# Performance work log

Hardware: AMD Instinct MI355X
Metric: run time of the kernel (lower is better)

## Reference

```python
import jax, jax.numpy as jnp
import numpy as np

N = 50000      # nodes
E = 800000     # edges (avg in-degree ~16)
IN = 64        # in_size
OUT = 64       # out_size
DELTA = 2.83   # PNA delta ~ log(avg_degree + 1)
MOM_EPS = 1e-30
BN_EPS = 1e-5


def setup_inputs() -> dict:
    key = jax.random.key(0)
    ks = jax.random.split(key, 8)
    node_feat = jax.random.normal(ks[0], (N, IN), dtype=jnp.float32)
    # Linear M: (2*IN -> IN); store weight as (2*IN, IN) for x @ W
    Wm = jax.random.normal(ks[1], (2 * IN, IN), dtype=jnp.float32) * (1.0 / np.sqrt(2 * IN))
    bm = jnp.zeros((IN,), jnp.float32)
    # Linear U: ((4 aggs * 3 scalers + 1) * IN -> OUT) = (13*IN -> OUT)
    Wu = jax.random.normal(ks[2], (13 * IN, OUT), dtype=jnp.float32) * (1.0 / np.sqrt(13 * IN))
    bu = jnp.zeros((OUT,), jnp.float32)
    gamma = jnp.ones((OUT,), jnp.float32)
    beta = jnp.zeros((OUT,), jnp.float32)
    src = jax.random.randint(ks[3], (E,), 0, N, dtype=jnp.int32)
    dst = jax.random.randint(ks[4], (E,), 0, N, dtype=jnp.int32)
    return {"node_feat": node_feat, "Wm": Wm, "bm": bm, "Wu": Wu, "bu": bu,
            "gamma": gamma, "beta": beta, "src": src, "dst": dst}


def _pna_forward(node_feat, Wm, bm, Wu, bu, gamma, beta, src, dst):
    # message MLP: M(h_src || h_dst) computed without materializing the concat
    msg = node_feat[src] @ Wm[:IN] + node_feat[dst] @ Wm[IN:] + bm  # (E, IN)

    deg = jax.ops.segment_sum(jnp.ones((E,), msg.dtype), dst, num_segments=N)  # (N,)
    safe_deg = jnp.maximum(deg, 1.0)[:, None]
    has_nbr = (deg > 0.0)[:, None]

    # multi-statistic ragged segment reduce
    s = jax.ops.segment_sum(msg, dst, num_segments=N)
    mean = s / safe_deg
    mean_sq = jax.ops.segment_sum(msg * msg, dst, num_segments=N) / safe_deg
    var = jax.nn.relu(mean_sq - mean * mean)
    std = jnp.sqrt(var + MOM_EPS)
    mx = jnp.where(has_nbr, jax.ops.segment_max(msg, dst, num_segments=N), 0.0)
    mn = jnp.where(has_nbr, jax.ops.segment_min(msg, dst, num_segments=N), 0.0)

    h = jnp.concatenate([mean, mx, mn, std], axis=1)  # (N, 4*IN)

    # scalers: identity, amplification log(D+1)/delta, attenuation delta/log(D+1)
    logD = jnp.log(deg + 1.0)[:, None]
    safe_logD = jnp.where(logD > 0.0, logD, 1.0)  # zero-degree rows masked below
    h_all = jnp.concatenate([h, h * (safe_logD / DELTA), h * (DELTA / safe_logD)], axis=1)
    h_neigh = jnp.where(has_nbr, h_all, 0.0)  # zero-degree nodes get 0 (DGL behavior)

    # update MLP + graph size norm (single graph: snorm = 1/sqrt(N))
    z = jnp.concatenate([node_feat, h_neigh], axis=1) @ Wu + bu  # (N, OUT)
    snorm = 1.0 / jnp.sqrt(jnp.asarray(N, z.dtype))
    z = z * snorm

    # BatchNorm1d, training mode (batch stats, biased variance)
    mu = jnp.mean(z, axis=0)
    v = jnp.mean((z - mu) ** 2, axis=0)
    return (z - mu) / jnp.sqrt(v + BN_EPS) * gamma + beta


def reference(node_feat, Wm, bm, Wu, bu, gamma, beta, src, dst):
    return _pna_forward(node_feat, Wm, bm, Wu, bu, gamma, beta, src, dst)
```

## Files before the change

### kernel.cpp

```cpp
#include <hip/hip_runtime.h>
#include <hip/hip_bf16.h>


#define DELTA_C 2.83f
#define BN_EPS_C 1e-5f
#define MOM_EPS_C 1e-30f
#define FLT_BIG 3.402823466e38f
#define BSHIFT 7
#define NBMAX 512

typedef __attribute__((ext_vector_type(8))) short bf16x8;
typedef __attribute__((ext_vector_type(4))) float f32x4;

static __device__ __forceinline__ unsigned short f2bf(float f) {
    unsigned u = __float_as_uint(f);
    unsigned r = (u + 0x7FFFu + ((u >> 16) & 1u)) >> 16;
    return (unsigned short)r;
}
static __device__ __forceinline__ unsigned pack2(float a, float b) {
    return (unsigned)f2bf(a) | ((unsigned)f2bf(b) << 16);
}
static __device__ __forceinline__ float bflo(unsigned u) { return __uint_as_float(u << 16); }
static __device__ __forceinline__ float bfhi(unsigned u) { return __uint_as_float(u & 0xFFFF0000u); }

__global__ __launch_bounds__(256) void repack_wu(
    const float* __restrict__ Wu, short* __restrict__ Wup,
    int* __restrict__ bcnt, float* __restrict__ bnacc)
{
    int t = threadIdx.x;
    if (blockIdx.x == 0) {
        bcnt[t] = 0; bcnt[t + 256] = 0;
        if (t < 128) bnacc[t] = 0.f;
    }
    int idx = blockIdx.x * 256 + t;
    int lane = idx & 63, c = (idx >> 6) & 3, kc = idx >> 8;
    int kbase = kc * 32 + (lane >> 4) * 8;
    int col = c * 16 + (lane & 15);
    unsigned short o[8];
    #pragma unroll
    for (int i = 0; i < 8; ++i)
        o[i] = f2bf(Wu[(size_t)(kbase + i) * 64 + col]);
    uint4 u;
    u.x = o[0] | ((unsigned)o[1] << 16);
    u.y = o[2] | ((unsigned)o[3] << 16);
    u.z = o[4] | ((unsigned)o[5] << 16);
    u.w = o[6] | ((unsigned)o[7] << 16);
    *(uint4*)(Wup + (size_t)idx * 8) = u;
}

__global__ __launch_bounds__(256) void proj_ab(
    const float* __restrict__ x, const float* __restrict__ Wm,
    unsigned* __restrict__ Ab, float* __restrict__ B,
    unsigned* __restrict__ xbu, int n,
    const int* __restrict__ dst, int* __restrict__ bcnt, int e, int nb_chunk)
{
    __shared__ float wm[128][68];
    __shared__ float xs[64][68];
    __shared__ int h[NBMAX];
    int t = threadIdx.x;
    for (int i = t; i < 2048; i += 256) {
        int k = i >> 4, c4 = (i & 15) << 2;
        *(float4*)&wm[k][c4] = *(const float4*)&Wm[k * 64 + c4];
    }
    int row0 = blockIdx.x * 64;
    for (int i = t; i < 1024; i += 256) {
        int r = i >> 4, k4 = (i & 15) << 2;
        int row = row0 + r;
        float4 v = make_float4(0.f, 0.f, 0.f, 0.f);
        if (row < n) v = *(const float4*)&x[(size_t)row * 64 + k4];
        *(float4*)&xs[r][k4] = v;
    }
    __syncthreads();
    int tr = t >> 4, tc = t & 15, c0 = tc << 2;
    float a[4][4] = {}; float b[4][4] = {};
    #pragma unroll 8
    for (int k = 0; k < 64; ++k) {
        float4 wa = *(float4*)&wm[k][c0];
        float4 wb = *(float4*)&wm[64 + k][c0];
        #pragma unroll
        for (int i = 0; i < 4; ++i) {
            float xv = xs[tr * 4 + i][k];
            a[i][0] += xv * wa.x; a[i][1] += xv * wa.y; a[i][2] += xv * wa.z; a[i][3] += xv * wa.w;
            b[i][0] += xv * wb.x; b[i][1] += xv * wb.y; b[i][2] += xv * wb.z; b[i][3] += xv * wb.w;
        }
    }
    #pragma unroll
    for (int i = 0; i < 4; ++i) {
        int r = tr * 4 + i;
        int row = row0 + r;
        uint2 xp;
        xp.x = pack2(xs[r][c0], xs[r][c0 + 1]);
        xp.y = pack2(xs[r][c0 + 2], xs[r][c0 + 3]);
        *(uint2*)&xbu[(size_t)row * 32 + (c0 >> 1)] = xp;
        if (row < n) {
            uint2 ap;
            ap.x = pack2(a[i][0], a[i][1]);
            ap.y = pack2(a[i][2], a[i][3]);
            *(uint2*)&Ab[(size_t)row * 32 + (c0 >> 1)] = ap;
            *(float4*)&B[(size_t)row * 64 + c0] = make_float4(b[i][0], b[i][1], b[i][2], b[i][3]);
        }
    }
    if (blockIdx.x < nb_chunk) {
        __syncthreads();
        for (int bb = t; bb < NBMAX; bb += 256) h[bb] = 0;
        __syncthreads();
        int base = blockIdx.x * 4096;
        int cnt = min(4096, e - base);
        for (int i = t; i < cnt; i += 256)
            atomicAdd(&h[dst[base + i] >> BSHIFT], 1);
        __syncthreads();
        for (int bb = t; bb < NBMAX; bb += 256)
            if (h[bb]) atomicAdd(&bcnt[bb], h[bb]);
    }
}

__global__ void bin_scan(const int* __restrict__ bcnt, int* __restrict__ boff,
                         int* __restrict__ gcur, int nb,
                         int* __restrict__ offs, int n, int e)
{
    int t = threadIdx.x;
    int v[8]; int s = 0;
    #pragma unroll
    for (int j = 0; j < 8; ++j) {
        int b = t * 8 + j;
        v[j] = (b < nb) ? bcnt[b] : 0;
        s += v[j];
    }
    int inc = s;
    #pragma unroll
    for (int st = 1; st < 64; st <<= 1) {
        int u = __shfl_up(inc, st);
        if (t >= st) inc += u;
    }
    int ex = inc - s;
    #pragma unroll
    for (int j = 0; j < 8; ++j) {
        int b = t * 8 + j;
        if (b < nb) { boff[b] = ex; gcur[b] = ex; }
        ex += v[j];
    }
    if (t == 63) { boff[nb] = e; offs[n] = e; }
}

__global__ __launch_bounds__(256) void bin_scatter(
    const int* __restrict__ src, const int* __restrict__ dst,
    int* __restrict__ gcur, unsigned* __restrict__ pairs_out, int e)
{
    __shared__ int hcnt[NBMAX], hstart[NBMAX], hcur[NBMAX], gpos[NBMAX];
    __shared__ unsigned pairs[4096];
    int t = threadIdx.x;
    int base = blockIdx.x * 4096;
    int cnt = min(4096, e - base);
    for (int b = t; b < NBMAX; b += 256) hcnt[b] = 0;
    __syncthreads();

    int ls[16], ld[16];
    #pragma unroll
    for (int j = 0; j < 16; ++j) {
        int i = t + j * 256;
        ls[j] = 0; ld[j] = -1;
        if (i < cnt) {
            ls[j] = src[base + i];
            ld[j] = dst[base + i];
            atomicAdd(&hcnt[ld[j] >> BSHIFT], 1);
        }
    }
    __syncthreads();
    if (t < 64) {
        int v[8]; int s = 0;
        #pragma unroll
        for (int j = 0; j < 8; ++j) { v[j] = hcnt[t * 8 + j]; s += v[j]; }
        int inc = s;
        #pragma unroll
        for (int st = 1; st < 64; st <<= 1) {
            int u = __shfl_up(inc, st);
            if (t >= st) inc += u;
        }
        int ex = inc - s;
        #pragma unroll
        for (int j = 0; j < 8; ++j) {
            hstart[t * 8 + j] = ex;
            hcur[t * 8 + j] = ex;
            ex += v[j];
        }
    }
    __syncthreads();
    #pragma unroll
    for (int j = 0; j < 16; ++j) {
        if (ld[j] >= 0) {
            int pos = atomicAdd(&hcur[ld[j] >> BSHIFT], 1);
            pairs[pos] = ((unsigned)ls[j] << 16) | (unsigned)ld[j];
        }
    }
    __syncthreads();
    for (int b = t; b < NBMAX; b += 256) {
        int c = hcnt[b];
        if (c) gpos[b] = atomicAdd(&gcur[b], c);
    }
    __syncthreads();
    #pragma unroll
    for (int j = 0; j < 16; ++j) {
        int i = t + j * 256;
        if (i < cnt) {
            unsigned p = pairs[i];
            int b = (int)(p & 0xFFFFu) >> BSHIFT;
            pairs_out[gpos[b] + (i - hstart[b])] = p;
        }
    }
}

__global__ __launch_bounds__(128) void csr_fill(
    const unsigned* __restrict__ pairs, const int* __restrict__ boff,
    int* __restrict__ offs, int* __restrict__ csr, int n)
{
    __shared__ int hist[128], pref[128], cur[128];
    int b = blockIdx.x, t = threadIdx.x;
    int base = boff[b], cnt = boff[b + 1] - base;
    int node0 = b << BSHIFT;
    hist[t] = 0;
    __syncthreads();
    for (int i = t; i < cnt; i += 128)
        atomicAdd(&hist[pairs[base + i] & 127u], 1);
    __syncthreads();
    if (t < 64) {
        int v0 = hist[2 * t], v1 = hist[2 * t + 1];
        int s = v0 + v1, inc = s;
        #pragma unroll
        for (int st = 1; st < 64; st <<= 1) {
            int u = __shfl_up(inc, st);
            if (t >= st) inc += u;
        }
        int ex = inc - s;
        pref[2 * t] = ex;       cur[2 * t] = ex;
        pref[2 * t + 1] = ex + v0; cur[2 * t + 1] = ex + v0;
    }
    __syncthreads();
    int node = node0 + t;
    if (node < n) offs[node] = base + pref[t];
    for (int i = t; i < cnt; i += 128) {
        unsigned p = pairs[base + i];
        int pos = atomicAdd(&cur[p & 127u], 1);
        csr[base + pos] = (int)(p >> 16);
    }
}

__global__ __launch_bounds__(256) void node_reduce(
    const unsigned* __restrict__ Ab, const float* __restrict__ Bp,
    const float* __restrict__ bm,
    const int* __restrict__ offs, const int* __restrict__ csr,
    unsigned* __restrict__ hbu, float* __restrict__ s1, float* __restrict__ s2,
    int n, int npad)
{
    int wid = threadIdx.x >> 6;
    int lane = threadIdx.x & 63;
    int node = blockIdx.x * 4 + wid;
    if (node >= npad) return;
    unsigned* hrow = hbu + (size_t)node * 128;
    int l32 = lane & 31;
    int half = lane >> 5;
    int beg = 0, dg = 0;
    if (node < n) { beg = offs[node]; dg = offs[node + 1] - beg; }
    if (dg == 0) {
        if (half == 0) {
            hrow[l32] = 0u; hrow[32 + l32] = 0u; hrow[64 + l32] = 0u; hrow[96 + l32] = 0u;
        }
        if (lane == 0) { s1[node] = 0.f; s2[node] = 0.f; }
        return;
    }

    float s0 = 0.f, s1a = 0.f, ss0 = 0.f, ss1 = 0.f;
    float mx0 = -FLT_BIG, mx1 = -FLT_BIG, mn0 = FLT_BIG, mn1 = FLT_BIG;

#define ACC(u) { float v0 = bflo(u), v1 = bfhi(u);                          \
    s0 += v0; s1a += v1;                                                    \
    ss0 = fmaf(v0, v0, ss0); ss1 = fmaf(v1, v1, ss1);                       \
    mx0 = fmaxf(mx0, v0); mx1 = fmaxf(mx1, v1);                             \
    mn0 = fminf(mn0, v0); mn1 = fminf(mn1, v1); }
#define GA(sel) Ab[(size_t)(sel) * 32 + l32]

    int j = beg, end = beg + dg;
    for (; j + 15 < end; j += 16) {
        int i0 = csr[j],      i1 = csr[j + 1],  i2 = csr[j + 2],  i3 = csr[j + 3];
        int i4 = csr[j + 4],  i5 = csr[j + 5],  i6 = csr[j + 6],  i7 = csr[j + 7];
        int i8 = csr[j + 8],  i9 = csr[j + 9],  i10 = csr[j + 10], i11 = csr[j + 11];
        int i12 = csr[j + 12], i13 = csr[j + 13], i14 = csr[j + 14], i15 = csr[j + 15];
        unsigned u0 = GA(half ? i1 : i0);
        unsigned u1 = GA(half ? i3 : i2);
        unsigned u2 = GA(half ? i5 : i4);
        unsigned u3 = GA(half ? i7 : i6);
        unsigned u4 = GA(half ? i9 : i8);
        unsigned u5 = GA(half ? i11 : i10);
        unsigned u6 = GA(half ? i13 : i12);
        unsigned u7 = GA(half ? i15 : i14);
        ACC(u0); ACC(u1); ACC(u2); ACC(u3);
        ACC(u4); ACC(u5); ACC(u6); ACC(u7);
    }
    for (; j + 7 < end; j += 8) {
        int i0 = csr[j],     i1 = csr[j + 1], i2 = csr[j + 2], i3 = csr[j + 3];
        int i4 = csr[j + 4], i5 = csr[j + 5], i6 = csr[j + 6], i7 = csr[j + 7];
        unsigned u0 = GA(half ? i1 : i0);
        unsigned u1 = GA(half ? i3 : i2);
        unsigned u2 = GA(half ? i5 : i4);
        unsigned u3 = GA(half ? i7 : i6);
        ACC(u0); ACC(u1); ACC(u2); ACC(u3);
    }
    for (; j + 1 < end; j += 2) {
        int i0 = csr[j], i1 = csr[j + 1];
        unsigned u0 = GA(half ? i1 : i0);
        ACC(u0);
    }
    if (j < end) {
        unsigned u0 = GA(csr[j]);
        if (half == 0) ACC(u0);
    }
#undef GA
#undef ACC

    s0 += __shfl_xor(s0, 32);  s1a += __shfl_xor(s1a, 32);
    ss0 += __shfl_xor(ss0, 32); ss1 += __shfl_xor(ss1, 32);
    mx0 = fmaxf(mx0, __shfl_xor(mx0, 32)); mx1 = fmaxf(mx1, __shfl_xor(mx1, 32));
    mn0 = fminf(mn0, __shfl_xor(mn0, 32)); mn1 = fminf(mn1, __shfl_xor(mn1, 32));

    float fd = (float)dg, inv = 1.0f / fd;
    float2 bv = *(const float2*)(Bp + (size_t)node * 64 + 2 * l32);
    float2 bmv = *(const float2*)(bm + 2 * l32);
    float bn0 = bv.x + bmv.x, bn1 = bv.y + bmv.y;
    float ma0 = s0 * inv, ma1 = s1a * inv;
    float var0 = ss0 * inv - ma0 * ma0; if (var0 < 0.f) var0 = 0.f;
    float var1 = ss1 * inv - ma1 * ma1; if (var1 < 0.f) var1 = 0.f;
    float sd0 = sqrtf(var0 + MOM_EPS_C), sd1 = sqrtf(var1 + MOM_EPS_C);

    if (half == 0) {
        hrow[l32]      = pack2(ma0 + bn0, ma1 + bn1);
        hrow[32 + l32] = pack2(mx0 + bn0, mx1 + bn1);
        hrow[64 + l32] = pack2(mn0 + bn0, mn1 + bn1);
        hrow[96 + l32] = pack2(sd0, sd1);
    }
    if (lane == 0) {
        float logD = logf(fd + 1.0f);
        s1[node] = logD / DELTA_C;
        s2[node] = DELTA_C / logD;
    }
}

__global__ __launch_bounds__(256) void gemm_mfma(
    const short* __restrict__ xb, const short* __restrict__ hb,
    const float* __restrict__ s1p, const float* __restrict__ s2p,
    const short* __restrict__ Wup, const float* __restrict__ bu,
    float* __restrict__ z, float* __restrict__ bnacc, int n, float snorm)
{
    __shared__ float bnl[4][2][64];
    int t = threadIdx.x;
    int lane = t & 63, w = t >> 6;
    int rb = blockIdx.x * 128 + w * 32;
    int r16 = lane & 15, kg = lane >> 4;

    f32x4 accx[2][4] = {};
    f32x4 acc1[2][4] = {};
    f32x4 acc2[2][4] = {};
    f32x4 acc3[2][4] = {};

    const short* xr0 = xb + (size_t)(rb + r16) * 64 + kg * 8;
    const short* xr1 = xr0 + 16 * 64;

    #pragma unroll
    for (int kc = 0; kc < 2; ++kc) {
        bf16x8 a0 = *(const bf16x8*)(xr0 + kc * 32);
        bf16x8 a1 = *(const bf16x8*)(xr1 + kc * 32);
        #pragma unroll
        for (int c = 0; c < 4; ++c) {
            bf16x8 b = *(const bf16x8*)(Wup + (size_t)((kc * 4 + c) * 64 + lane) * 8);
            accx[0][c] = __builtin_amdgcn_mfma_f32_16x16x32_bf16(a0, b, accx[0][c], 0, 0, 0);
            accx[1][c] = __builtin_amdgcn_mfma_f32_16x16x32_bf16(a1, b, accx[1][c], 0, 0, 0);
        }
    }

    const short* hr0 = hb + (size_t)(rb + r16) * 256 + kg * 8;
    const short* hr1 = hr0 + 16 * 256;

    #pragma unroll 1
    for (int kh = 0; kh < 8; ++kh) {
        bf16x8 a0 = *(const bf16x8*)(hr0 + kh * 32);
        bf16x8 a1 = *(const bf16x8*)(hr1 + kh * 32);
        #pragma unroll
        for (int c = 0; c < 4; ++c) {
            bf16x8 b1 = *(const bf16x8*)(Wup + (size_t)(((2  + kh) * 4 + c) * 64 + lane) * 8);
            bf16x8 b2 = *(const bf16x8*)(Wup + (size_t)(((10 + kh) * 4 + c) * 64 + lane) * 8);
            bf16x8 b3 = *(const bf16x8*)(Wup + (size_t)(((18 + kh) * 4 + c) * 64 + lane) * 8);
            acc1[0][c] = __builtin_amdgcn_mfma_f32_16x16x32_bf16(a0, b1, acc1[0][c], 0, 0, 0);
            acc1[1][c] = __builtin_amdgcn_mfma_f32_16x16x32_bf16(a1, b1, acc1[1][c], 0, 0, 0);
            acc2[0][c] = __builtin_amdgcn_mfma_f32_16x16x32_bf16(a0, b2, acc2[0][c], 0, 0, 0);
            acc2[1][c] = __builtin_amdgcn_mfma_f32_16x16x32_bf16(a1, b2, acc2[1][c], 0, 0, 0);
            acc3[0][c] = __builtin_amdgcn_mfma_f32_16x16x32_bf16(a0, b3, acc3[0][c], 0, 0, 0);
            acc3[1][c] = __builtin_amdgcn_mfma_f32_16x16x32_bf16(a1, b3, acc3[1][c], 0, 0, 0);
        }
    }

    float cs[4] = {}, css[4] = {};
    #pragma unroll
    for (int s = 0; s < 2; ++s) {
        int r0 = rb + s * 16 + kg * 4;
        float s1v[4], s2v[4];
        #pragma unroll
        for (int r = 0; r < 4; ++r) { s1v[r] = s1p[r0 + r]; s2v[r] = s2p[r0 + r]; }
        #pragma unroll
        for (int c = 0; c < 4; ++c) {
            int col = c * 16 + r16;
            float bval = bu[col];
            #pragma unroll
            for (int r = 0; r < 4; ++r) {
                int row = r0 + r;
                if (row < n) {
                    float v = (accx[s][c][r] + acc1[s][c][r]
                            + s1v[r] * acc2[s][c][r] + s2v[r] * acc3[s][c][r] + bval) * snorm;
                    z[(size_t)row * 64 + col] = v;
                    cs[c] += v;
                    css[c] = fmaf(v, v, css[c]);
                }
            }
        }
    }
    #pragma unroll
    for (int c = 0; c < 4; ++c) {
        float a = cs[c];  a += __shfl_xor(a, 16); a += __shfl_xor(a, 32); cs[c] = a;
        float b = css[c]; b += __shfl_xor(b, 16); b += __shfl_xor(b, 32); css[c] = b;
    }
    if (lane < 16) {
        #pragma unroll
        for (int c = 0; c < 4; ++c) {
            bnl[w][0][c * 16 + lane] = cs[c];
            bnl[w][1][c * 16 + lane] = css[c];
        }
    }
    __syncthreads();
    if (t < 128) {
        int st = t >> 6, cc = t & 63;
        float tot = bnl[0][st][cc] + bnl[1][st][cc] + bnl[2][st][cc] + bnl[3][st][cc];
        atomicAdd(&bnacc[st * 64 + cc], tot);
    }
}

__global__ __launch_bounds__(256) void bn_apply(
    float* __restrict__ z, const float* __restrict__ acc,
    const float* __restrict__ gamma, const float* __restrict__ beta, int n)
{
    float inv_n = 1.0f / (float)n;
    int tid = blockIdx.x * 256 + threadIdx.x;
    int c0 = (tid * 4) & 63;
    float sc[4], sh[4];
    #pragma unroll
    for (int k = 0; k < 4; ++k) {
        int c = c0 + k;
        float mu = acc[c] * inv_n;
        float var = acc[64 + c] * inv_n - mu * mu;
        if (var < 0.f) var = 0.f;
        float inv = rsqrtf(var + BN_EPS_C) * gamma[c];
        sc[k] = inv;
        sh[k] = beta[c] - mu * inv;
    }
    int total4 = n * 16;
    int stride = gridDim.x * 256;
    for (int i = tid; i < total4; i += stride) {
        float4 v = *(float4*)&z[(size_t)i * 4];
        v.x = fmaf(v.x, sc[0], sh[0]);
        v.y = fmaf(v.y, sc[1], sh[1]);
        v.z = fmaf(v.z, sc[2], sh[2]);
        v.w = fmaf(v.w, sc[3], sh[3]);
        *(float4*)&z[(size_t)i * 4] = v;
    }
}

extern "C" void kernel_launch(void* const* d_in, const int* in_sizes, int n_in,
                              void* d_out, int out_size, void* d_ws, size_t ws_size,
                              hipStream_t stream)
{
    const float* x     = (const float*)d_in[0];
    const float* Wm    = (const float*)d_in[1];
    const float* bm    = (const float*)d_in[2];
    const float* Wu    = (const float*)d_in[3];
    const float* bu    = (const float*)d_in[4];
    const float* gamma = (const float*)d_in[5];
    const float* beta  = (const float*)d_in[6];
    const int*   src   = (const int*)d_in[7];
    const int*   dst   = (const int*)d_in[8];

    int n = in_sizes[0] / 64;
    int e = in_sizes[7];
    int npad = ((n + 127) / 128) * 128;
    int nb = (n + 127) >> BSHIFT;
    float* z = (float*)d_out;

    char* w = (char*)d_ws;
    size_t off = 0;
    auto take = [&](size_t bytes) -> void* {
        void* p = w + off;
        off = (off + bytes + 255) & ~(size_t)255;
        return p;
    };
    unsigned* Ab    = (unsigned*)take((size_t)npad * 32 * sizeof(unsigned));
    float*    B     = (float*)take((size_t)n * 64 * sizeof(float));
    unsigned* xbu   = (unsigned*)take((size_t)npad * 32 * sizeof(unsigned));
    unsigned* hbu   = (unsigned*)take((size_t)npad * 128 * sizeof(unsigned));
    float*    s1    = (float*)take((size_t)npad * sizeof(float));
    float*    s2    = (float*)take((size_t)npad * sizeof(float));
    short*    Wup   = (short*)take((size_t)26 * 4 * 64 * 8 * sizeof(short));
    int*      offs  = (int*)take((size_t)(n + 1) * sizeof(int));
    int*      csr   = (int*)take((size_t)e * sizeof(int));
    unsigned* prs   = (unsigned*)take((size_t)e * sizeof(unsigned));
    int*      bcnt  = (int*)take((size_t)NBMAX * sizeof(int));
    int*      boff  = (int*)take((size_t)(NBMAX + 1) * sizeof(int));
    int*      gcur  = (int*)take((size_t)NBMAX * sizeof(int));
    float*    bnacc = (float*)take(128 * sizeof(float));

    (void)n_in; (void)out_size; (void)ws_size;

    int nb_rows64 = npad / 64;
    int nb_chunk = (e + 4095) / 4096;

    repack_wu<<<26, 256, 0, stream>>>(Wu, Wup, bcnt, bnacc);
    proj_ab<<<nb_rows64, 256, 0, stream>>>(x, Wm, Ab, B, xbu, n, dst, bcnt, e, nb_chunk);
    bin_scan<<<1, 64, 0, stream>>>(bcnt, boff, gcur, nb, offs, n, e);
    bin_scatter<<<nb_chunk, 256, 0, stream>>>(src, dst, gcur, prs, e);
    csr_fill<<<nb, 128, 0, stream>>>(prs, boff, offs, csr, n);
    node_reduce<<<(npad + 3) / 4, 256, 0, stream>>>(Ab, B, bm, offs, csr, hbu, s1, s2, n, npad);

    float snorm = (float)(1.0 / sqrt((double)n));
    gemm_mfma<<<npad / 128, 256, 0, stream>>>((const short*)xbu, (const short*)hbu,
                                              s1, s2, Wup, bu, z, bnacc, n, snorm);

    bn_apply<<<512, 256, 0, stream>>>(z, bnacc, gamma, beta, n);
}
```

Before: 123.3 us.

## Fold bin scan into scatter/fill kernels and widen node_reduce gathers to 16B

Removes the single-block bin_scan launch: bin_scatter now computes the bin prefix sums redundantly per block from bcnt, and gcur becomes a zero-initialized relative cursor. csr_fill computes its base offset by summing the preceding bin counts and writes the final offs entry itself. node_reduce is restructured so each lane loads a uint4 (8 bf16 values) per neighbor, with 8 neighbors handled concurrently per wavefront, followed by a cross-group shuffle reduction. This trades one kernel launch and narrow 4-byte gathers for redundant scan work in every block and more registers per thread.

```diff
diff --git a/kernel.cpp b/kernel.cpp
--- a/kernel.cpp
+++ b/kernel.cpp
@@ -25,11 +25,12 @@
 
 __global__ __launch_bounds__(256) void repack_wu(
     const float* __restrict__ Wu, short* __restrict__ Wup,
-    int* __restrict__ bcnt, float* __restrict__ bnacc)
+    int* __restrict__ bcnt, int* __restrict__ gcur, float* __restrict__ bnacc)
 {
     int t = threadIdx.x;
     if (blockIdx.x == 0) {
         bcnt[t] = 0; bcnt[t + 256] = 0;
+        gcur[t] = 0; gcur[t + 256] = 0;
         if (t < 128) bnacc[t] = 0.f;
     }
     int idx = blockIdx.x * 256 + t;
@@ -114,44 +115,37 @@
     }
 }
 
-__global__ void bin_scan(const int* __restrict__ bcnt, int* __restrict__ boff,
-                         int* __restrict__ gcur, int nb,
-                         int* __restrict__ offs, int n, int e)
-{
-    int t = threadIdx.x;
-    int v[8]; int s = 0;
-    #pragma unroll
-    for (int j = 0; j < 8; ++j) {
-        int b = t * 8 + j;
-        v[j] = (b < nb) ? bcnt[b] : 0;
-        s += v[j];
-    }
-    int inc = s;
-    #pragma unroll
-    for (int st = 1; st < 64; st <<= 1) {
-        int u = __shfl_up(inc, st);
-        if (t >= st) inc += u;
-    }
-    int ex = inc - s;
-    #pragma unroll
-    for (int j = 0; j < 8; ++j) {
-        int b = t * 8 + j;
-        if (b < nb) { boff[b] = ex; gcur[b] = ex; }
-        ex += v[j];
-    }
-    if (t == 63) { boff[nb] = e; offs[n] = e; }
-}
-
 __global__ __launch_bounds__(256) void bin_scatter(
     const int* __restrict__ src, const int* __restrict__ dst,
-    int* __restrict__ gcur, unsigned* __restrict__ pairs_out, int e)
-{
-    __shared__ int hcnt[NBMAX], hstart[NBMAX], hcur[NBMAX], gpos[NBMAX];
+    const int* __restrict__ bcnt, int* __restrict__ gcur,
+    unsigned* __restrict__ pairs_out, int e)
+{
+    __shared__ int hcnt[NBMAX], hstart[NBMAX], hcur[NBMAX], gpos[NBMAX], sgoff[NBMAX];
     __shared__ unsigned pairs[4096];
     int t = threadIdx.x;
     int base = blockIdx.x * 4096;
     int cnt = min(4096, e - base);
     for (int b = t; b < NBMAX; b += 256) hcnt[b] = 0;
+    if (t < 64) {
+        int v0 = bcnt[t * 8],     v1 = bcnt[t * 8 + 1], v2 = bcnt[t * 8 + 2], v3 = bcnt[t * 8 + 3];
+        int v4 = bcnt[t * 8 + 4], v5 = bcnt[t * 8 + 5], v6 = bcnt[t * 8 + 6], v7 = bcnt[t * 8 + 7];
+        int s = v0 + v1 + v2 + v3 + v4 + v5 + v6 + v7;
+        int inc = s;
+        #pragma unroll
+        for (int st = 1; st < 64; st <<= 1) {
+            int u = __shfl_up(inc, st);
+            if (t >= st) inc += u;
+        }
+        int ex = inc - s;
+        sgoff[t * 8] = ex;         ex += v0;
+        sgoff[t * 8 + 1] = ex;     ex += v1;
+        sgoff[t * 8 + 2] = ex;     ex += v2;
+        sgoff[t * 8 + 3] = ex;     ex += v3;
+        sgoff[t * 8 + 4] = ex;     ex += v4;
+        sgoff[t * 8 + 5] = ex;     ex += v5;
+        sgoff[t * 8 + 6] = ex;     ex += v6;
+        sgoff[t * 8 + 7] = ex;
+    }
     __syncthreads();
 
     int ls[16], ld[16];
@@ -195,7 +189,7 @@
     __syncthreads();
     for (int b = t; b < NBMAX; b += 256) {
         int c = hcnt[b];
-        if (c) gpos[b] = atomicAdd(&gcur[b], c);
+        if (c) gpos[b] = sgoff[b] + atomicAdd(&gcur[b], c);
     }
     __syncthreads();
     #pragma unroll
@@ -210,15 +204,23 @@
 }
 
 __global__ __launch_bounds__(128) void csr_fill(
-    const unsigned* __restrict__ pairs, const int* __restrict__ boff,
-    int* __restrict__ offs, int* __restrict__ csr, int n)
-{
-    __shared__ int hist[128], pref[128], cur[128];
+    const unsigned* __restrict__ pairs, const int* __restrict__ bcnt,
+    int* __restrict__ offs, int* __restrict__ csr, int n, int e)
+{
+    __shared__ int hist[128], pref[128], cur[128], sbase[1];
     int b = blockIdx.x, t = threadIdx.x;
-    int base = boff[b], cnt = boff[b + 1] - base;
+    if (t < 64) {
+        int acc = 0;
+        for (int k = t; k < b; k += 64) acc += bcnt[k];
+        acc += __shfl_down(acc, 32); acc += __shfl_down(acc, 16);
+        acc += __shfl_down(acc, 8);  acc += __shfl_down(acc, 4);
+        acc += __shfl_down(acc, 2);  acc += __shfl_down(acc, 1);
+        if (t == 0) sbase[0] = acc;
+    }
+    hist[t] = 0;
+    __syncthreads();
+    int base = sbase[0], cnt = bcnt[b];
     int node0 = b << BSHIFT;
-    hist[t] = 0;
-    __syncthreads();
     for (int i = t; i < cnt; i += 128)
         atomicAdd(&hist[pairs[base + i] & 127u], 1);
     __syncthreads();
@@ -237,6 +239,7 @@
     __syncthreads();
     int node = node0 + t;
     if (node < n) offs[node] = base + pref[t];
+    if (b == gridDim.x - 1 && t == 0) offs[n] = e;
     for (int i = t; i < cnt; i += 128) {
         unsigned p = pairs[base + i];
         int pos = atomicAdd(&cur[p & 127u], 1);
@@ -256,87 +259,106 @@
     int node = blockIdx.x * 4 + wid;
     if (node >= npad) return;
     unsigned* hrow = hbu + (size_t)node * 128;
-    int l32 = lane & 31;
-    int half = lane >> 5;
+    int g = lane >> 3;
+    int q = lane & 7;
     int beg = 0, dg = 0;
     if (node < n) { beg = offs[node]; dg = offs[node + 1] - beg; }
     if (dg == 0) {
-        if (half == 0) {
-            hrow[l32] = 0u; hrow[32 + l32] = 0u; hrow[64 + l32] = 0u; hrow[96 + l32] = 0u;
+        if (lane < 8) {
+            uint4 zz = make_uint4(0u, 0u, 0u, 0u);
+            *(uint4*)&hrow[q * 4]      = zz;
+            *(uint4*)&hrow[32 + q * 4] = zz;
+            *(uint4*)&hrow[64 + q * 4] = zz;
+            *(uint4*)&hrow[96 + q * 4] = zz;
         }
         if (lane == 0) { s1[node] = 0.f; s2[node] = 0.f; }
         return;
     }
 
-    float s0 = 0.f, s1a = 0.f, ss0 = 0.f, ss1 = 0.f;
-    float mx0 = -FLT_BIG, mx1 = -FLT_BIG, mn0 = FLT_BIG, mn1 = FLT_BIG;
-
-#define ACC(u) { float v0 = bflo(u), v1 = bfhi(u);                          \
-    s0 += v0; s1a += v1;                                                    \
-    ss0 = fmaf(v0, v0, ss0); ss1 = fmaf(v1, v1, ss1);                       \
-    mx0 = fmaxf(mx0, v0); mx1 = fmaxf(mx1, v1);                             \
-    mn0 = fminf(mn0, v0); mn1 = fminf(mn1, v1); }
-#define GA(sel) Ab[(size_t)(sel) * 32 + l32]
+    float as0 = 0.f, as1 = 0.f, as2 = 0.f, as3 = 0.f, as4 = 0.f, as5 = 0.f, as6 = 0.f, as7 = 0.f;
+    float aq0 = 0.f, aq1 = 0.f, aq2 = 0.f, aq3 = 0.f, aq4 = 0.f, aq5 = 0.f, aq6 = 0.f, aq7 = 0.f;
+    float ax0 = -FLT_BIG, ax1 = -FLT_BIG, ax2 = -FLT_BIG, ax3 = -FLT_BIG,
+          ax4 = -FLT_BIG, ax5 = -FLT_BIG, ax6 = -FLT_BIG, ax7 = -FLT_BIG;
+    float am0 = FLT_BIG, am1 = FLT_BIG, am2 = FLT_BIG, am3 = FLT_BIG,
+          am4 = FLT_BIG, am5 = FLT_BIG, am6 = FLT_BIG, am7 = FLT_BIG;
+
+#define ACCP(u, S0, Q0, X0, M0, S1_, Q1_, X1_, M1_) {                         \
+    float v0 = bflo(u), v1 = bfhi(u);                                         \
+    S0 += v0; Q0 = fmaf(v0, v0, Q0); X0 = fmaxf(X0, v0); M0 = fminf(M0, v0);  \
+    S1_ += v1; Q1_ = fmaf(v1, v1, Q1_); X1_ = fmaxf(X1_, v1); M1_ = fminf(M1_, v1); }
+#define ACC8(V) {                                          \
+    ACCP((V).x, as0, aq0, ax0, am0, as1, aq1, ax1, am1);   \
+    ACCP((V).y, as2, aq2, ax2, am2, as3, aq3, ax3, am3);   \
+    ACCP((V).z, as4, aq4, ax4, am4, as5, aq5, ax5, am5);   \
+    ACCP((V).w, as6, aq6, ax6, am6, as7, aq7, ax7, am7); }
+#define GA4(idx) (((const uint4*)Ab)[(size_t)(idx) * 8 + q])
 
     int j = beg, end = beg + dg;
     for (; j + 15 < end; j += 16) {
-        int i0 = csr[j],      i1 = csr[j + 1],  i2 = csr[j + 2],  i3 = csr[j + 3];
-        int i4 = csr[j + 4],  i5 = csr[j + 5],  i6 = csr[j + 6],  i7 = csr[j + 7];
-        int i8 = csr[j + 8],  i9 = csr[j + 9],  i10 = csr[j + 10], i11 = csr[j + 11];
-        int i12 = csr[j + 12], i13 = csr[j + 13], i14 = csr[j + 14], i15 = csr[j + 15];
-        unsigned u0 = GA(half ? i1 : i0);
-        unsigned u1 = GA(half ? i3 : i2);
-        unsigned u2 = GA(half ? i5 : i4);
-        unsigned u3 = GA(half ? i7 : i6);
-        unsigned u4 = GA(half ? i9 : i8);
-        unsigned u5 = GA(half ? i11 : i10);
-        unsigned u6 = GA(half ? i13 : i12);
-        unsigned u7 = GA(half ? i15 : i14);
-        ACC(u0); ACC(u1); ACC(u2); ACC(u3);
-        ACC(u4); ACC(u5); ACC(u6); ACC(u7);
+        int ia = csr[j + g];
+        int ib = csr[j + 8 + g];
+        uint4 va = GA4(ia);
+        uint4 vb = GA4(ib);
+        ACC8(va); ACC8(vb);
     }
     for (; j + 7 < end; j += 8) {
-        int i0 = csr[j],     i1 = csr[j + 1], i2 = csr[j + 2], i3 = csr[j + 3];
-        int i4 = csr[j + 4], i5 = csr[j + 5], i6 = csr[j + 6], i7 = csr[j + 7];
-        unsigned u0 = GA(half ? i1 : i0);
-        unsigned u1 = GA(half ? i3 : i2);
-        unsigned u2 = GA(half ? i5 : i4);
-        unsigned u3 = GA(half ? i7 : i6);
-        ACC(u0); ACC(u1); ACC(u2); ACC(u3);
-    }
-    for (; j + 1 < end; j += 2) {
-        int i0 = csr[j], i1 = csr[j + 1];
-        unsigned u0 = GA(half ? i1 : i0);
-        ACC(u0);
+        int ia = csr[j + g];
+        uint4 va = GA4(ia);
+        ACC8(va);
     }
     if (j < end) {
-        unsigned u0 = GA(csr[j]);
-        if (half == 0) ACC(u0);
-    }
-#undef GA
-#undef ACC
-
-    s0 += __shfl_xor(s0, 32);  s1a += __shfl_xor(s1a, 32);
-    ss0 += __shfl_xor(ss0, 32); ss1 += __shfl_xor(ss1, 32);
-    mx0 = fmaxf(mx0, __shfl_xor(mx0, 32)); mx1 = fmaxf(mx1, __shfl_xor(mx1, 32));
-    mn0 = fminf(mn0, __shfl_xor(mn0, 32)); mn1 = fminf(mn1, __shfl_xor(mn1, 32));
-
-    float fd = (float)dg, inv = 1.0f / fd;
-    float2 bv = *(const float2*)(Bp + (size_t)node * 64 + 2 * l32);
-    float2 bmv = *(const float2*)(bm + 2 * l32);
-    float bn0 = bv.x + bmv.x, bn1 = bv.y + bmv.y;
-    float ma0 = s0 * inv, ma1 = s1a * inv;
-    float var0 = ss0 * inv - ma0 * ma0; if (var0 < 0.f) var0 = 0.f;
-    float var1 = ss1 * inv - ma1 * ma1; if (var1 < 0.f) var1 = 0.f;
-    float sd0 = sqrtf(var0 + MOM_EPS_C), sd1 = sqrtf(var1 + MOM_EPS_C);
-
-    if (half == 0) {
-        hrow[l32]      = pack2(ma0 + bn0, ma1 + bn1);
-        hrow[32 + l32] = pack2(mx0 + bn0, mx1 + bn1);
-        hrow[64 + l32] = pack2(mn0 + bn0, mn1 + bn1);
-        hrow[96 + l32] = pack2(sd0, sd1);
+        int jp = j + g; if (jp > end - 1) jp = end - 1;
+        int ia = csr[jp];
+        uint4 va = GA4(ia);
+        if (j + g < end) ACC8(va);
+    }
+#undef GA4
+#undef ACC8
+#undef ACCP
+
+#define RSUM(a) { a += __shfl_xor(a, 8); a += __shfl_xor(a, 16); a += __shfl_xor(a, 32); }
+#define RMAX(a) { a = fmaxf(a, __shfl_xor(a, 8)); a = fmaxf(a, __shfl_xor(a, 16)); a = fmaxf(a, __shfl_xor(a, 32)); }
+#define RMIN(a) { a = fminf(a, __shfl_xor(a, 8)); a = fminf(a, __shfl_xor(a, 16)); a = fminf(a, __shfl_xor(a, 32)); }
+    RSUM(as0); RSUM(as1); RSUM(as2); RSUM(as3); RSUM(as4); RSUM(as5); RSUM(as6); RSUM(as7);
+    RSUM(aq0); RSUM(aq1); RSUM(aq2); RSUM(aq3); RSUM(aq4); RSUM(aq5); RSUM(aq6); RSUM(aq7);
+    RMAX(ax0); RMAX(ax1); RMAX(ax2); RMAX(ax3); RMAX(ax4); RMAX(ax5); RMAX(ax6); RMAX(ax7);
+    RMIN(am0); RMIN(am1); RMIN(am2); RMIN(am3); RMIN(am4); RMIN(am5); RMIN(am6); RMIN(am7);
+#undef RSUM
+#undef RMAX
+#undef RMIN
+
+    if (lane < 8) {
+        float fd = (float)dg, inv = 1.0f / fd;
+        float4 bA = *(const float4*)(Bp + (size_t)node * 64 + q * 8);
+        float4 bB = *(const float4*)(Bp + (size_t)node * 64 + q * 8 + 4);
+        float4 mA = *(const float4*)(bm + q * 8);
+        float4 mB = *(const float4*)(bm + q * 8 + 4);
+        float bn0 = bA.x + mA.x, bn1 = bA.y + mA.y, bn2 = bA.z + mA.z, bn3 = bA.w + mA.w;
+        float bn4 = bB.x + mB.x, bn5 = bB.y + mB.y, bn6 = bB.z + mB.z, bn7 = bB.w + mB.w;
+#define FIN(S, Q, ME, SD) { ME = S * inv; float vv = Q * inv - ME * ME;       \
+    if (vv < 0.f) vv = 0.f; SD = sqrtf(vv + MOM_EPS_C); }
+        float me0, me1, me2, me3, me4, me5, me6, me7;
+        float sd0, sd1, sd2, sd3, sd4, sd5, sd6, sd7;
+        FIN(as0, aq0, me0, sd0); FIN(as1, aq1, me1, sd1);
+        FIN(as2, aq2, me2, sd2); FIN(as3, aq3, me3, sd3);
+        FIN(as4, aq4, me4, sd4); FIN(as5, aq5, me5, sd5);
+        FIN(as6, aq6, me6, sd6); FIN(as7, aq7, me7, sd7);
+#undef FIN
+        uint4 wmean = make_uint4(pack2(me0 + bn0, me1 + bn1), pack2(me2 + bn2, me3 + bn3),
+                                 pack2(me4 + bn4, me5 + bn5), pack2(me6 + bn6, me7 + bn7));
+        uint4 wmax  = make_uint4(pack2(ax0 + bn0, ax1 + bn1), pack2(ax2 + bn2, ax3 + bn3),
+                                 pack2(ax4 + bn4, ax5 + bn5), pack2(ax6 + bn6, ax7 + bn7));
+        uint4 wmin  = make_uint4(pack2(am0 + bn0, am1 + bn1), pack2(am2 + bn2, am3 + bn3),
+                                 pack2(am4 + bn4, am5 + bn5), pack2(am6 + bn6, am7 + bn7));
+        uint4 wstd  = make_uint4(pack2(sd0, sd1), pack2(sd2, sd3),
+                                 pack2(sd4, sd5), pack2(sd6, sd7));
+        *(uint4*)&hrow[q * 4]      = wmean;
+        *(uint4*)&hrow[32 + q * 4] = wmax;
+        *(uint4*)&hrow[64 + q * 4] = wmin;
+        *(uint4*)&hrow[96 + q * 4] = wstd;
     }
     if (lane == 0) {
+        float fd = (float)dg;
         float logD = logf(fd + 1.0f);
         s1[node] = logD / DELTA_C;
         s2[node] = DELTA_C / logD;
@@ -508,7 +530,6 @@
     int*      csr   = (int*)take((size_t)e * sizeof(int));
     unsigned* prs   = (unsigned*)take((size_t)e * sizeof(unsigned));
     int*      bcnt  = (int*)take((size_t)NBMAX * sizeof(int));
-    int*      boff  = (int*)take((size_t)(NBMAX + 1) * sizeof(int));
     int*      gcur  = (int*)take((size_t)NBMAX * sizeof(int));
     float*    bnacc = (float*)take(128 * sizeof(float));
 
@@ -517,11 +538,10 @@
     int nb_rows64 = npad / 64;
     int nb_chunk = (e + 4095) / 4096;
 
-    repack_wu<<<26, 256, 0, stream>>>(Wu, Wup, bcnt, bnacc);
+    repack_wu<<<26, 256, 0, stream>>>(Wu, Wup, bcnt, gcur, bnacc);
     proj_ab<<<nb_rows64, 256, 0, stream>>>(x, Wm, Ab, B, xbu, n, dst, bcnt, e, nb_chunk);
-    bin_scan<<<1, 64, 0, stream>>>(bcnt, boff, gcur, nb, offs, n, e);
-    bin_scatter<<<nb_chunk, 256, 0, stream>>>(src, dst, gcur, prs, e);
-    csr_fill<<<nb, 128, 0, stream>>>(prs, boff, offs, csr, n);
+    bin_scatter<<<nb_chunk, 256, 0, stream>>>(src, dst, bcnt, gcur, prs, e);
+    csr_fill<<<nb, 128, 0, stream>>>(prs, bcnt, offs, csr, n, e);
     node_reduce<<<(npad + 3) / 4, 256, 0, stream>>>(Ab, B, bm, offs, csr, hbu, s1, s2, n, npad);
 
     float snorm = (float)(1.0 / sqrt((double)n));
```

New measurement: 149.5 us. +21.3%, slower.
